# Kernel optimization log

Hardware: AMD Instinct MI355X
Metric: run time of the kernel (lower is better)

## Reference

```python
import jax, jax.numpy as jnp
import numpy as np

ALPHA = 0.01  # ema_decay

def setup_inputs() -> dict:
    key = jax.random.key(0)
    k1, k2 = jax.random.split(key)
    B, S, H = 8, 2048, 2048
    x = jax.random.normal(k1, (B, S, H), dtype=jnp.float32)
    W = jax.random.normal(k2, (H, H), dtype=jnp.float32) * (1.0 / np.sqrt(H))
    b = jnp.zeros((H,), dtype=jnp.float32)
    return {"x": x, "W": W, "b": b}

def reference(x, W, b):
    B, S, H = x.shape
    dt = x.dtype
    # p = [S-1, S-2, ..., 0]; w_prime = (1-alpha)^p
    p = jnp.arange(S - 1, -1, -1, dtype=dt)
    one_m_a = jnp.asarray(1.0 - ALPHA, dtype=dt)
    w_prime = one_m_a ** p                                   # [S]
    # w = w_prime, but positions t>=1 scaled by alpha
    w = jnp.where(jnp.arange(S) >= 1, w_prime * ALPHA, w_prime)  # [S]
    c = jnp.cumsum(x * w[None, :, None], axis=1)             # [B,S,H]
    s = c / w_prime[None, :, None]                           # [B,S,H]
    # nn.Linear: s @ W^T + b
    return jnp.einsum('bsh,oh->bso', s, W) + b
```

## Files before the change

### kernel.cpp

```cpp
#include <hip/hip_runtime.h>
#include <cstdint>
#include <cstddef>

#define ALPHA 0.01f
#define A1    0.99f
#define B_    8
#define S_    2048
#define H_    2048
#define NCH   16
#define CL    128
#define NKT   32

typedef __attribute__((ext_vector_type(8))) short bf16x8;
typedef __attribute__((ext_vector_type(4))) float f32x4;

__device__ __forceinline__ unsigned short f2bf(float f) {
    unsigned int u = __float_as_uint(f);
    u += 0x7FFFu + ((u >> 16) & 1u);
    return (unsigned short)(u >> 16);
}

__device__ __forceinline__ void gld16(const void* g, void* l) {
    __builtin_amdgcn_global_load_lds(
        (const __attribute__((address_space(1))) unsigned int*)g,
        (__attribute__((address_space(3))) unsigned int*)l, 16, 0, 0);
}

__global__ void ema_cast_w(const float* __restrict__ W, short* __restrict__ Wb) {
    int i = (blockIdx.x * 256 + threadIdx.x) * 4;
    float4 v = *(const float4*)(W + i);
    short4 o;
    o.x = (short)f2bf(v.x);
    o.y = (short)f2bf(v.y);
    o.z = (short)f2bf(v.z);
    o.w = (short)f2bf(v.w);
    *(short4*)(Wb + i) = o;
}

__global__ __launch_bounds__(256) void ema_carry_kernel(
        const float* __restrict__ x, float* __restrict__ carry) {
    int bid = blockIdx.x;
    int hg = bid & 3;
    int c  = (bid >> 2) & 15;
    int b  = bid >> 6;
    int h0 = (hg << 9) + (threadIdx.x << 1);
    const float2* px = (const float2*)(x + ((size_t)(b * S_) + (size_t)c * CL) * H_ + h0);
    const int STR = H_ / 2;
    float s0, s1;
    int i0;
    if (c == 0) { float2 v = px[0]; s0 = v.x; s1 = v.y; i0 = 1; }
    else        { s0 = 0.f; s1 = 0.f;                   i0 = 0; }
    #pragma unroll 8
    for (int i = i0; i < CL; ++i) {
        float2 v = px[(size_t)i * STR];
        s0 = fmaf(A1, s0, ALPHA * v.x);
        s1 = fmaf(A1, s1, ALPHA * v.y);
    }
    *(float2*)(carry + ((b << 4) + c) * H_ + h0) = (float2){s0, s1};
}

__global__ __launch_bounds__(256) void ema_apply_kernel(
        const float* __restrict__ x, const float* __restrict__ carry,
        unsigned short* __restrict__ sb) {
    int bid = blockIdx.x;
    int hg = bid & 3;
    int c  = (bid >> 2) & 15;
    int b  = bid >> 6;
    int h0 = (hg << 9) + (threadIdx.x << 1);

    float A128 = A1;
    #pragma unroll
    for (int q = 0; q < 7; ++q) A128 *= A128;

    float c0 = 0.f, c1 = 0.f, f = 1.f;
    for (int j = c - 1; j >= 0; --j) {
        float2 cv = *(const float2*)(carry + ((b << 4) + j) * H_ + h0);
        c0 = fmaf(cv.x, f, c0);
        c1 = fmaf(cv.y, f, c1);
        f *= A128;
    }

    size_t base = ((size_t)(b * S_) + (size_t)c * CL) * H_ + h0;
    const float2* px = (const float2*)(x + base);
    unsigned int*  pu = (unsigned int*)(sb + base);
    const int STR = H_ / 2;
    float s0, s1;
    int i0;
    if (c == 0) {
        float2 v = px[0]; s0 = v.x; s1 = v.y;
        pu[0] = (unsigned int)f2bf(s0) | ((unsigned int)f2bf(s1) << 16);
        i0 = 1;
    } else { s0 = c0; s1 = c1; i0 = 0; }
    #pragma unroll 8
    for (int i = i0; i < CL; ++i) {
        float2 v = px[(size_t)i * STR];
        s0 = fmaf(A1, s0, ALPHA * v.x);
        s1 = fmaf(A1, s1, ALPHA * v.y);
        pu[(size_t)i * STR] = (unsigned int)f2bf(s0) | ((unsigned int)f2bf(s1) << 16);
    }
}


#define BAR __builtin_amdgcn_s_barrier()
#define VMW(n) asm volatile("s_waitcnt vmcnt(" #n ")" ::: "memory")

#define STGA(i, kt, buf) gld16(gA[i] + (size_t)(kt) * 128, &ldsA[buf][((i) << 12) + (w << 9)])
#define STGB(i, kt, buf) gld16(gB[i] + (size_t)(kt) * 128, &ldsB[buf][((i) << 12) + (w << 9)])

#define LDA(dst, mh) do { int ra_ = (wm << 1) | (mh);                              \
    const char* base_ = (const char*)&ldsA[cur][0]                                 \
        + (((((ra_ & 1) << 1) | (ra_ >> 1))) << 13) + laneRow;                     \
    _Pragma("unroll") for (int m_ = 0; m_ < 4; ++m_) {                             \
        dst[m_][0] = *(const bf16x8*)(base_ + (m_ << 11) + ck0);                   \
        dst[m_][1] = *(const bf16x8*)(base_ + (m_ << 11) + ck1); } } while (0)

#define LDB(nh) do { const char* base_ = (const char*)&ldsB[cur][0]                \
        + ((nh) << 14) + (wn << 12) + laneRow;                                     \
    _Pragma("unroll") for (int n_ = 0; n_ < 2; ++n_) {                             \
        Bf[(nh) * 2 + n_][0] = *(const bf16x8*)(base_ + (n_ << 11) + ck0);         \
        Bf[(nh) * 2 + n_][1] = *(const bf16x8*)(base_ + (n_ << 11) + ck1); } } while (0)

#define MM(Asrc, mh, nh) do { __builtin_amdgcn_s_setprio(1);                       \
    _Pragma("unroll") for (int m_ = 0; m_ < 4; ++m_)                               \
    _Pragma("unroll") for (int n_ = 0; n_ < 2; ++n_)                               \
    _Pragma("unroll") for (int k_ = 0; k_ < 2; ++k_)                               \
        acc[(mh) * 4 + m_][(nh) * 2 + n_] = __builtin_amdgcn_mfma_f32_16x16x32_bf16( \
            Asrc[m_][k_], Bf[(nh) * 2 + n_][k_], acc[(mh) * 4 + m_][(nh) * 2 + n_], 0, 0, 0); \
    __builtin_amdgcn_s_setprio(0); } while (0)

__global__ __launch_bounds__(512, 2) void ema_gemm_kernel(
        const short* __restrict__ Sb, const short* __restrict__ Wb,
        const float* __restrict__ bias, float* __restrict__ out) {
    __shared__ short ldsA[2][16384];
    __shared__ short ldsB[2][16384];

    int bid = blockIdx.x;
    int swz = ((bid & 7) << 6) | (bid >> 3);
    int tm = swz >> 3;
    int tn = swz & 7;

    int tid  = threadIdx.x;
    int lane = tid & 63;
    int w    = tid >> 6;
    int wm   = w >> 2;
    int wn   = w & 3;

    const int K2 = H_ * 2;
    int rowA = tm << 8;
    int rowB = tn << 8;

    int rowoff = (w << 3) + (lane >> 3);
    int colb   = (((lane & 7) ^ (lane >> 3)) << 4);
    const char* SbB = (const char*)Sb;
    const char* WbB = (const char*)Wb;
    const char* gA[4];
    const char* gB[4];
    #pragma unroll
    for (int i = 0; i < 4; ++i) {
        int lq = ((i & 1) << 1) | (i >> 1);
        gA[i] = SbB + (size_t)(rowA + lq * 64 + rowoff) * K2 + colb;
        int pos = 2 * i + (w >> 2);
        int ls  = ((pos & 3) << 1) | (pos >> 2);
        gB[i] = WbB + (size_t)(rowB + ls * 32 + ((w & 3) << 3) + (lane >> 3)) * K2 + colb;
    }

    int laneRow = (lane & 15) << 7;
    int ck0 = (((lane >> 4)) ^ (lane & 7)) << 4;
    int ck1 = ((4 + (lane >> 4)) ^ (lane & 7)) << 4;

    f32x4 acc[8][4];
    #pragma unroll
    for (int i = 0; i < 8; ++i)
        #pragma unroll
        for (int j = 0; j < 4; ++j)
            acc[i][j] = (f32x4){0.f, 0.f, 0.f, 0.f};
    bf16x8 Af0[4][2], Af1[4][2], Bf[4][2];

    int colg = (tn << 8) + (wn << 6) + (lane & 15);
    float bb[4];
    #pragma unroll
    for (int n = 0; n < 4; ++n) bb[n] = bias[colg + (n << 4)];

    STGA(0, 0, 0); STGA(1, 0, 0); STGB(0, 0, 0); STGB(1, 0, 0);
    STGA(2, 0, 0); STGA(3, 0, 0); STGB(2, 0, 0); STGB(3, 0, 0);
    STGA(0, 1, 1); STGA(1, 1, 1); STGB(0, 1, 1); STGB(1, 1, 1);
    VMW(6);
    BAR;

    for (int t = 0; t < NKT; ++t) {
        int cur = t & 1, nxt = cur ^ 1;
        bool i01 = (t < NKT - 1), i23 = (t < NKT - 2);
        LDA(Af0, 0); LDB(0);
        if (i01) { STGA(2, t + 1, nxt); STGA(3, t + 1, nxt); VMW(6); }
        BAR;
        MM(Af0, 0, 0);
        LDB(1);
        if (i01) { STGB(2, t + 1, nxt); STGB(3, t + 1, nxt); }
        BAR;
        MM(Af0, 0, 1);
        LDA(Af1, 1);
        if (i23) { STGA(0, t + 2, cur); STGA(1, t + 2, cur); }
        BAR;
        MM(Af1, 1, 0);
        if (i23)                { STGB(0, t + 2, cur); STGB(1, t + 2, cur); VMW(6); }
        else if (t == NKT - 2)  { VMW(0); }
        BAR;
        MM(Af1, 1, 1);
    }

    int rowg = (tm << 8) + (wm << 7) + ((lane >> 4) << 2);
    #pragma unroll
    for (int m = 0; m < 8; ++m) {
        #pragma unroll
        for (int n = 0; n < 4; ++n) {
            int c = colg + (n << 4);
            size_t rb = (size_t)(rowg + (m << 4)) << 11;
            #pragma unroll
            for (int q = 0; q < 4; ++q)
                out[rb + ((size_t)q << 11) + c] = acc[m][n][q] + bb[n];
        }
    }
}

extern "C" void kernel_launch(void* const* d_in, const int* in_sizes, int n_in,
                              void* d_out, int out_size, void* d_ws, size_t ws_size,
                              hipStream_t stream) {
    const float* x    = (const float*)d_in[0];
    const float* W    = (const float*)d_in[1];
    const float* bias = (const float*)d_in[2];
    float* out = (float*)d_out;

    char* ws = (char*)d_ws;
    size_t s_bytes = (size_t)B_ * S_ * H_ * 2;
    size_t w_bytes = (size_t)H_ * H_ * 2;
    unsigned short* s_bf  = (unsigned short*)ws;
    short*          w_bf  = (short*)(ws + s_bytes);
    float*          carry = (float*)(ws + s_bytes + w_bytes);

    ema_cast_w<<<(H_ * H_) / 1024, 256, 0, stream>>>(W, w_bf);
    ema_carry_kernel<<<B_ * NCH * (H_ / 512), 256, 0, stream>>>(x, carry);
    ema_apply_kernel<<<B_ * NCH * (H_ / 512), 256, 0, stream>>>(x, carry, s_bf);
    ema_gemm_kernel<<<(16384 / 256) * (2048 / 256), 512, 0, stream>>>(
        (const short*)s_bf, w_bf, bias, out);
}
```

Baseline: 182.4 us.

## Use 4 waves per GEMM block with 128x128 per-wave tiles

```diff
diff --git a/kernel.cpp b/kernel.cpp
--- a/kernel.cpp
+++ b/kernel.cpp
@@ -104,8 +104,12 @@
 #define BAR __builtin_amdgcn_s_barrier()
 #define VMW(n) asm volatile("s_waitcnt vmcnt(" #n ")" ::: "memory")
 
-#define STGA(i, kt, buf) gld16(gA[i] + (size_t)(kt) * 128, &ldsA[buf][((i) << 12) + (w << 9)])
-#define STGB(i, kt, buf) gld16(gB[i] + (size_t)(kt) * 128, &ldsB[buf][((i) << 12) + (w << 9)])
+#define STGA(i, kt, buf) do {                                                      \
+    gld16(gA[i] + (size_t)(kt) * 128,            &ldsA[buf][((i) << 12) + (w << 9)]); \
+    gld16(gA[i] + (size_t)(kt) * 128 + 32 * K2,  &ldsA[buf][((i) << 12) + 2048 + (w << 9)]); } while (0)
+#define STGB(i, kt, buf) do {                                                      \
+    gld16(gB[i] + (size_t)(kt) * 128,            &ldsB[buf][((i) << 12) + (w << 9)]); \
+    gld16(gB[i] + (size_t)(kt) * 128 + 32 * K2,  &ldsB[buf][((i) << 12) + 2048 + (w << 9)]); } while (0)
 
 #define LDA(dst, mh) do { int ra_ = (wm << 1) | (mh);                              \
     const char* base_ = (const char*)&ldsA[cur][0]                                 \
@@ -114,21 +118,21 @@
         dst[m_][0] = *(const bf16x8*)(base_ + (m_ << 11) + ck0);                   \
         dst[m_][1] = *(const bf16x8*)(base_ + (m_ << 11) + ck1); } } while (0)
 
-#define LDB(nh) do { const char* base_ = (const char*)&ldsB[cur][0]                \
-        + ((nh) << 14) + (wn << 12) + laneRow;                                     \
-    _Pragma("unroll") for (int n_ = 0; n_ < 2; ++n_) {                             \
-        Bf[(nh) * 2 + n_][0] = *(const bf16x8*)(base_ + (n_ << 11) + ck0);         \
-        Bf[(nh) * 2 + n_][1] = *(const bf16x8*)(base_ + (n_ << 11) + ck1); } } while (0)
-
-#define MM(Asrc, mh, nh) do { __builtin_amdgcn_s_setprio(1);                       \
+#define LDB(dst, nh) do { int sl_ = (wn << 1) | (nh);                              \
+    const char* base_ = (const char*)&ldsB[cur][0] + (sl_ << 13) + laneRow;        \
+    _Pragma("unroll") for (int n_ = 0; n_ < 4; ++n_) {                             \
+        dst[n_][0] = *(const bf16x8*)(base_ + (n_ << 11) + ck0);                   \
+        dst[n_][1] = *(const bf16x8*)(base_ + (n_ << 11) + ck1); } } while (0)
+
+#define MM(Asrc, Bsrc, mh, nh) do { __builtin_amdgcn_s_setprio(1);                 \
     _Pragma("unroll") for (int m_ = 0; m_ < 4; ++m_)                               \
-    _Pragma("unroll") for (int n_ = 0; n_ < 2; ++n_)                               \
+    _Pragma("unroll") for (int n_ = 0; n_ < 4; ++n_)                               \
     _Pragma("unroll") for (int k_ = 0; k_ < 2; ++k_)                               \
-        acc[(mh) * 4 + m_][(nh) * 2 + n_] = __builtin_amdgcn_mfma_f32_16x16x32_bf16( \
-            Asrc[m_][k_], Bf[(nh) * 2 + n_][k_], acc[(mh) * 4 + m_][(nh) * 2 + n_], 0, 0, 0); \
+        acc[(mh) * 4 + m_][(nh) * 4 + n_] = __builtin_amdgcn_mfma_f32_16x16x32_bf16( \
+            Asrc[m_][k_], Bsrc[n_][k_], acc[(mh) * 4 + m_][(nh) * 4 + n_], 0, 0, 0); \
     __builtin_amdgcn_s_setprio(0); } while (0)
 
-__global__ __launch_bounds__(512, 2) void ema_gemm_kernel(
+__global__ __launch_bounds__(256, 1) void ema_gemm_kernel(
         const short* __restrict__ Sb, const short* __restrict__ Wb,
         const float* __restrict__ bias, float* __restrict__ out) {
     __shared__ short ldsA[2][16384];
@@ -142,8 +146,8 @@
     int tid  = threadIdx.x;
     int lane = tid & 63;
     int w    = tid >> 6;
-    int wm   = w >> 2;
-    int wn   = w & 3;
+    int wm   = w >> 1;
+    int wn   = w & 1;
 
     const int K2 = H_ * 2;
     int rowA = tm << 8;
@@ -159,60 +163,58 @@
     for (int i = 0; i < 4; ++i) {
         int lq = ((i & 1) << 1) | (i >> 1);
         gA[i] = SbB + (size_t)(rowA + lq * 64 + rowoff) * K2 + colb;
-        int pos = 2 * i + (w >> 2);
-        int ls  = ((pos & 3) << 1) | (pos >> 2);
-        gB[i] = WbB + (size_t)(rowB + ls * 32 + ((w & 3) << 3) + (lane >> 3)) * K2 + colb;
+        gB[i] = WbB + (size_t)(rowB + i * 64 + rowoff) * K2 + colb;
     }
 
     int laneRow = (lane & 15) << 7;
     int ck0 = (((lane >> 4)) ^ (lane & 7)) << 4;
     int ck1 = ((4 + (lane >> 4)) ^ (lane & 7)) << 4;
 
-    f32x4 acc[8][4];
+    f32x4 acc[8][8];
     #pragma unroll
     for (int i = 0; i < 8; ++i)
         #pragma unroll
-        for (int j = 0; j < 4; ++j)
+        for (int j = 0; j < 8; ++j)
             acc[i][j] = (f32x4){0.f, 0.f, 0.f, 0.f};
-    bf16x8 Af0[4][2], Af1[4][2], Bf[4][2];
-
-    int colg = (tn << 8) + (wn << 6) + (lane & 15);
-    float bb[4];
-    #pragma unroll
-    for (int n = 0; n < 4; ++n) bb[n] = bias[colg + (n << 4)];
-
-    STGA(0, 0, 0); STGA(1, 0, 0); STGB(0, 0, 0); STGB(1, 0, 0);
-    STGA(2, 0, 0); STGA(3, 0, 0); STGB(2, 0, 0); STGB(3, 0, 0);
-    STGA(0, 1, 1); STGA(1, 1, 1); STGB(0, 1, 1); STGB(1, 1, 1);
-    VMW(6);
+    bf16x8 Af0[4][2], Af1[4][2], Bf0[4][2], Bf1[4][2];
+
+    int colg = (tn << 8) + (wn << 7) + (lane & 15);
+    float bb[8];
+    #pragma unroll
+    for (int n = 0; n < 8; ++n) bb[n] = bias[colg + (n << 4)];
+
+    STGA(0, 0, 0); STGA(1, 0, 0); STGB(0, 0, 0); STGB(2, 0, 0);
+    STGA(2, 0, 0); STGA(3, 0, 0); STGB(1, 0, 0); STGB(3, 0, 0);
+    STGA(0, 1, 1); STGA(1, 1, 1); STGB(0, 1, 1); STGB(2, 1, 1);
+    VMW(12);
     BAR;
 
     for (int t = 0; t < NKT; ++t) {
         int cur = t & 1, nxt = cur ^ 1;
         bool i01 = (t < NKT - 1), i23 = (t < NKT - 2);
-        LDA(Af0, 0); LDB(0);
-        if (i01) { STGA(2, t + 1, nxt); STGA(3, t + 1, nxt); VMW(6); }
-        BAR;
-        MM(Af0, 0, 0);
-        LDB(1);
-        if (i01) { STGB(2, t + 1, nxt); STGB(3, t + 1, nxt); }
-        BAR;
-        MM(Af0, 0, 1);
+        LDA(Af0, 0); LDB(Bf0, 0);
+        if (i01) { STGA(2, t + 1, nxt); STGA(3, t + 1, nxt); VMW(12); }
+        BAR;
+        MM(Af0, Bf0, 0, 0);
+        LDB(Bf1, 1);
+        if (i01) { STGB(1, t + 1, nxt); STGB(3, t + 1, nxt); }
+        BAR;
+        MM(Af0, Bf1, 0, 1);
         LDA(Af1, 1);
         if (i23) { STGA(0, t + 2, cur); STGA(1, t + 2, cur); }
         BAR;
-        MM(Af1, 1, 0);
-        if (i23)                { STGB(0, t + 2, cur); STGB(1, t + 2, cur); VMW(6); }
+        MM(Af1, Bf0, 1, 0);
+        if (i23)                { STGB(0, t + 2, cur); STGB(2, t + 2, cur); VMW(12); }
         else if (t == NKT - 2)  { VMW(0); }
         BAR;
-        MM(Af1, 1, 1);
+        MM(Af1, Bf1, 1, 1);
     }
 
     int rowg = (tm << 8) + (wm << 7) + ((lane >> 4) << 2);
     #pragma unroll
     for (int m = 0; m < 8; ++m) {
         #pragma unroll
-        for (int n = 0; n < 4; ++n) {
+        for (int n = 0; n < 8; ++n) {
             int c = colg + (n << 4);
             size_t rb = (size_t)(rowg + (m << 4)) << 11;
             #pragma unroll
@@ -240,6 +242,6 @@
     ema_cast_w<<<(H_ * H_) / 1024, 256, 0, stream>>>(W, w_bf);
     ema_carry_kernel<<<B_ * NCH * (H_ / 512), 256, 0, stream>>>(x, carry);
     ema_apply_kernel<<<B_ * NCH * (H_ / 512), 256, 0, stream>>>(x, carry, s_bf);
-    ema_gemm_kernel<<<(16384 / 256) * (2048 / 256), 512, 0, stream>>>(
+    ema_gemm_kernel<<<(16384 / 256) * (2048 / 256), 256, 0, stream>>>(
         (const short*)s_bf, w_bf, bias, out);
 }
```

New measurement: 199.5 us. 1.09x slower.
